# Kernel tuning notes

Measured on AMD Instinct MI355X. Metric: run time of the kernel, lower is better.

The kernel has to match this reference:

```python
import jax, jax.numpy as jnp
import numpy as np

NUM_SCALES = 3
LAMBDA_0 = 1.0
MU_0 = 1.0
KAPPA_LAMBDA = 0.5
KAPPA_MU = 0.5
BASE_WEIGHT = 1.0
GRADIENT_SCALING = 0.1


def tgradient(f, axis):
    """torch.gradient semantics: central diff interior, one-sided at edges (spacing=1)."""
    n = f.shape[axis]
    def sl(a, b):
        idx = [slice(None)] * f.ndim
        idx[axis] = slice(a, b)
        return f[tuple(idx)]
    interior = (sl(2, n) - sl(0, n - 2)) * 0.5
    first = sl(1, 2) - sl(0, 1)
    last = sl(n - 1, n) - sl(n - 2, n - 1)
    return jnp.concatenate([first, interior, last], axis=axis)


def resize1d_linear(x, axis, out_size):
    """1D linear resize along `axis` with align_corners=True."""
    in_size = x.shape[axis]
    if out_size == in_size:
        return x
    denom = max(out_size - 1, 1)
    coords = jnp.arange(out_size, dtype=jnp.float32) * ((in_size - 1) / denom)
    i0 = jnp.floor(coords).astype(jnp.int32)
    i1 = jnp.minimum(i0 + 1, in_size - 1)
    w = (coords - i0.astype(jnp.float32)).astype(x.dtype)
    shape = [1] * x.ndim
    shape[axis] = out_size
    w = w.reshape(shape)
    x0 = jnp.take(x, i0, axis=axis)
    x1 = jnp.take(x, i1, axis=axis)
    return x0 * (1 - w) + x1 * w


def trilinear_downsample(x, scale):
    # F.interpolate(..., scale_factor=1/scale, mode='trilinear', align_corners=True,
    # recompute_scale_factor=True): out_size = floor(in_size / scale); separable linear.
    for axis in (2, 3, 4):
        out_size = int(np.floor(x.shape[axis] / scale))
        x = resize1d_linear(x, axis, out_size)
    return x


def elasticity_loss(deformation_field, image):
    total_loss = jnp.float32(0.0)
    for i in range(NUM_SCALES):
        scale = 2 ** i
        deform = trilinear_downsample(deformation_field, scale)
        img = trilinear_downsample(image, scale)
        u, v, w = deform[:, 0], deform[:, 1], deform[:, 2]  # each (B, X, Y, Z)
        du_dx, du_dy, du_dz = tgradient(u, 1), tgradient(u, 2), tgradient(u, 3)
        dv_dx, dv_dy, dv_dz = tgradient(v, 1), tgradient(v, 2), tgradient(v, 3)
        dw_dx, dw_dy, dw_dz = tgradient(w, 1), tgradient(w, 2), tgradient(w, 3)
        E_xx, E_yy, E_zz = du_dx, dv_dy, dw_dz
        E_xy = 0.5 * (du_dy + dv_dx)
        E_xz = 0.5 * (du_dz + dw_dx)
        E_yz = 0.5 * (dv_dz + dw_dy)
        trace_E = E_xx + E_yy + E_zz
        ic = img[:, 0]  # (B, X, Y, Z)
        gx, gy, gz = tgradient(ic, 1), tgradient(ic, 2), tgradient(ic, 3)
        image_gradient = jnp.sqrt(gx * gx + gy * gy + gz * gz)
        adaptive_lambda = LAMBDA_0 + KAPPA_LAMBDA * image_gradient
        adaptive_mu = MU_0 + KAPPA_MU * image_gradient
        elastic_energy = (0.5 * adaptive_lambda * trace_E ** 2
                          + adaptive_mu * (E_xx ** 2 + E_yy ** 2 + E_zz ** 2
                                           + 2.0 * (E_xy ** 2 + E_xz ** 2 + E_yz ** 2)))
        adaptive_weight = BASE_WEIGHT + GRADIENT_SCALING * image_gradient
        total_loss = total_loss + jnp.mean(adaptive_weight * elastic_energy)
    return total_loss


def setup_inputs() -> dict:
    key = jax.random.key(0)
    k1, k2 = jax.random.split(key)
    deformation_field = jax.random.normal(k1, (2, 3, 160, 192, 160), dtype=jnp.float32)
    image = jax.random.uniform(k2, (2, 1, 160, 192, 160), dtype=jnp.float32)
    return {"deformation_field": deformation_field, "image": image}


def reference(deformation_field, image):
    return elasticity_loss(deformation_field, image)
```

## Files before the change

kernel.cpp:

```cpp
#include <hip/hip_runtime.h>
#include <math.h>


#define LAMBDA_0 1.0f
#define MU_0 1.0f
#define KAPPA_LAMBDA 0.5f
#define KAPPA_MU 0.5f
#define BASE_WEIGHT 1.0f
#define GRADIENT_SCALING 0.1f

typedef float v4f __attribute__((ext_vector_type(4)));

constexpr int S_TY = 32;
constexpr int S_TZ = 32;
constexpr int S_CX = 8;

__global__ __launch_bounds__(256, 2)
void elasticity_stream_reg2_kernel(const float* __restrict__ def,
                                   const float* __restrict__ img,
                                   int X, int Y, int Z,
                                   int nby, int nbz, int nbx,
                                   float inv_n, float* __restrict__ out) {
    int t = blockIdx.x;
    const int bx = t % nbx; t /= nbx;
    const int bz = t % nbz; t /= nbz;
    const int by = t % nby; t /= nby;
    const int b = t;

    const int tid = threadIdx.x;
    const int zg = tid & 7;
    const int ly = tid >> 3;
    const int lane = tid & 63;
    const int laneM = (lane - 1) & 63;
    const int laneP = (lane + 1) & 63;

    const long long vol = (long long)X * Y * Z;
    const long long sX = (long long)Y * Z;
    const float* __restrict__ p0 = def + ((long long)b * 3 + 0) * vol;
    const float* __restrict__ p1 = def + ((long long)b * 3 + 1) * vol;
    const float* __restrict__ p2 = def + ((long long)b * 3 + 2) * vol;
    const float* __restrict__ p3 = img + (long long)b * vol;

    const int gy = by * S_TY + ly;
    const int gz0 = bz * S_TZ + 4 * zg;
    const int x0 = bx * S_CX;

    const long long offC  = (long long)gy * Z + gz0;
    const long long offYm = (long long)max(gy - 1, 0) * Z + gz0;
    const long long offYp = (long long)min(gy + 1, Y - 1) * Z + gz0;
    const long long offZm = offC - ((gz0 > 0) ? 1 : 0);
    const long long offZp = offC + ((gz0 + 4 < Z) ? 4 : 3);

    const bool ylo = (gy == 0), yhi = (gy == Y - 1);
    const bool zlo = (gz0 == 0), zhi = (gz0 + 4 == Z);
    const bool zem = (zg == 0),  zep = (zg == 7);

    v4f pc[4], cc[4], nc[4];
    {
        const long long o_ = (long long)max(x0 - 1, 0) * sX;
        pc[0] = *(const v4f*)(p0 + o_ + offC);
        pc[1] = *(const v4f*)(p1 + o_ + offC);
        pc[2] = *(const v4f*)(p2 + o_ + offC);
        pc[3] = *(const v4f*)(p3 + o_ + offC);
    }
    {
        const long long o_ = (long long)x0 * sX;
        cc[0] = *(const v4f*)(p0 + o_ + offC);
        cc[1] = *(const v4f*)(p1 + o_ + offC);
        cc[2] = *(const v4f*)(p2 + o_ + offC);
        cc[3] = *(const v4f*)(p3 + o_ + offC);
    }

    float acc = 0.f;
#pragma unroll 2
    for (int i = 0; i < S_CX; ++i) {
        const int x = x0 + i;
        const bool xlo = (x == 0), xhi = (x == X - 1);
        const long long oC = (long long)x * sX;
        const long long oN = (long long)min(x + 1, X - 1) * sX;

        nc[0] = *(const v4f*)(p0 + oN + offC);
        nc[1] = *(const v4f*)(p1 + oN + offC);
        nc[2] = *(const v4f*)(p2 + oN + offC);
        nc[3] = *(const v4f*)(p3 + oN + offC);

        v4f ym[4], yp[4];
        ym[0] = *(const v4f*)(p0 + oC + offYm);
        ym[1] = *(const v4f*)(p1 + oC + offYm);
        ym[2] = *(const v4f*)(p2 + oC + offYm);
        ym[3] = *(const v4f*)(p3 + oC + offYm);
        yp[0] = *(const v4f*)(p0 + oC + offYp);
        yp[1] = *(const v4f*)(p1 + oC + offYp);
        yp[2] = *(const v4f*)(p2 + oC + offYp);
        yp[3] = *(const v4f*)(p3 + oC + offYp);

        float zmS[4] = {0.f, 0.f, 0.f, 0.f};
        float zpS[4] = {0.f, 0.f, 0.f, 0.f};
        if (zem) {
            zmS[0] = p0[oC + offZm]; zmS[1] = p1[oC + offZm];
            zmS[2] = p2[oC + offZm]; zmS[3] = p3[oC + offZm];
        }
        if (zep) {
            zpS[0] = p0[oC + offZp]; zpS[1] = p1[oC + offZp];
            zpS[2] = p2[oC + offZp]; zpS[3] = p3[oC + offZp];
        }

        v4f gxA[4], gyA[4], gzA[4];
#pragma unroll
        for (int f = 0; f < 4; ++f) {
            v4f c = cc[f];
            gxA[f] = xlo ? (nc[f] - c)
                         : (xhi ? (c - pc[f]) : 0.5f * (nc[f] - pc[f]));
            gyA[f] = ylo ? (yp[f] - c)
                         : (yhi ? (c - ym[f]) : 0.5f * (yp[f] - ym[f]));
            float zmv = __shfl(c[3], laneM, 64);
            float zpv = __shfl(c[0], laneP, 64);
            float zm = zem ? zmS[f] : zmv;
            float zp = zep ? zpS[f] : zpv;
            v4f gz;
            gz[0] = zlo ? (c[1] - c[0]) : 0.5f * (c[1] - zm);
            gz[1] = 0.5f * (c[2] - c[0]);
            gz[2] = 0.5f * (c[3] - c[1]);
            gz[3] = zhi ? (c[3] - c[2]) : 0.5f * (zp - c[2]);
            gzA[f] = gz;
        }

#pragma unroll
        for (int j = 0; j < 4; ++j) {
            float Exx = gxA[0][j], Eyy = gyA[1][j], Ezz = gzA[2][j];
            float Exy = 0.5f * (gyA[0][j] + gxA[1][j]);
            float Exz = 0.5f * (gzA[0][j] + gxA[2][j]);
            float Eyz = 0.5f * (gzA[1][j] + gyA[2][j]);
            float tr = Exx + Eyy + Ezz;
            float g = sqrtf(gxA[3][j] * gxA[3][j] + gyA[3][j] * gyA[3][j] +
                            gzA[3][j] * gzA[3][j]);
            float lam = LAMBDA_0 + KAPPA_LAMBDA * g;
            float mu  = MU_0 + KAPPA_MU * g;
            float energy = 0.5f * lam * tr * tr +
                           mu * (Exx * Exx + Eyy * Eyy + Ezz * Ezz +
                                 2.0f * (Exy * Exy + Exz * Exz + Eyz * Eyz));
            acc += (BASE_WEIGHT + GRADIENT_SCALING * g) * energy;
        }

#pragma unroll
        for (int f = 0; f < 4; ++f) { pc[f] = cc[f]; cc[f] = nc[f]; }
    }

    float val = acc * inv_n;
    for (int off = 32; off > 0; off >>= 1)
        val += __shfl_down(val, off, 64);
    __shared__ float smem[4];
    const int wid = (int)(threadIdx.x >> 6);
    if ((threadIdx.x & 63) == 0) smem[wid] = val;
    __syncthreads();
    if (threadIdx.x == 0)
        atomicAdd(out, smem[0] + smem[1] + smem[2] + smem[3]);
}


__global__ void downsample3d_kernel(const float* __restrict__ in,
                                    float* __restrict__ out,
                                    int nmaps,
                                    int inX, int inY, int inZ,
                                    int outX, int outY, int outZ,
                                    float rx, float ry, float rz) {
    long long total = (long long)nmaps * outX * outY * outZ;
    long long idx = (long long)blockIdx.x * blockDim.x + threadIdx.x;
    if (idx >= total) return;

    int z = (int)(idx % outZ);
    long long t = idx / outZ;
    int y = (int)(t % outY);
    t /= outY;
    int x = (int)(t % outX);
    int m = (int)(t / outX);

    float cx = (float)x * rx;
    float cy = (float)y * ry;
    float cz = (float)z * rz;
    int ix0 = (int)floorf(cx), iy0 = (int)floorf(cy), iz0 = (int)floorf(cz);
    float wx = cx - (float)ix0, wy = cy - (float)iy0, wz = cz - (float)iz0;
    int ix1 = min(ix0 + 1, inX - 1);
    int iy1 = min(iy0 + 1, inY - 1);
    int iz1 = min(iz0 + 1, inZ - 1);

    long long sYZ = (long long)inY * inZ;
    const float* p = in + (long long)m * inX * sYZ;

    long long bx0 = (long long)ix0 * sYZ, bx1 = (long long)ix1 * sYZ;
    long long by0 = (long long)iy0 * inZ, by1 = (long long)iy1 * inZ;

    float v000 = p[bx0 + by0 + iz0], v001 = p[bx0 + by0 + iz1];
    float v010 = p[bx0 + by1 + iz0], v011 = p[bx0 + by1 + iz1];
    float v100 = p[bx1 + by0 + iz0], v101 = p[bx1 + by0 + iz1];
    float v110 = p[bx1 + by1 + iz0], v111 = p[bx1 + by1 + iz1];

    float a00 = v000 * (1.f - wx) + v100 * wx;
    float a01 = v001 * (1.f - wx) + v101 * wx;
    float a10 = v010 * (1.f - wx) + v110 * wx;
    float a11 = v011 * (1.f - wx) + v111 * wx;
    float b0 = a00 * (1.f - wy) + a10 * wy;
    float b1 = a01 * (1.f - wy) + a11 * wy;
    out[idx] = b0 * (1.f - wz) + b1 * wz;
}

__global__ void elasticity_loss_v4_kernel(const float* __restrict__ def,
                                          const float* __restrict__ img,
                                          int B, int X, int Y, int Z,
                                          float inv_n,
                                          float* __restrict__ out) {
    const int Zg = Z >> 2;
    long long total = (long long)B * X * Y * Zg;
    long long idx = (long long)blockIdx.x * blockDim.x + threadIdx.x;
    float val = 0.f;
    if (idx < total) {
        int zg = (int)(idx % Zg);
        long long t = idx / Zg;
        int y = (int)(t % Y);
        t /= Y;
        int x = (int)(t % X);
        int b = (int)(t / X);
        int z0 = zg << 2;

        long long vol = (long long)X * Y * Z;
        const float* base0 = def + ((long long)b * 3 + 0) * vol;
        const float* base1 = def + ((long long)b * 3 + 1) * vol;
        const float* base2 = def + ((long long)b * 3 + 2) * vol;
        const float* base3 = img + (long long)b * vol;
        const float* bases[4] = {base0, base1, base2, base3};

        long long sX = (long long)Y * Z;
        long long c = (long long)x * sX + (long long)y * Z + z0;
        long long cxm = (x > 0) ? c - sX : c;
        long long cxp = (x < X - 1) ? c + sX : c;
        long long cym = (y > 0) ? c - Z : c;
        long long cyp = (y < Y - 1) ? c + Z : c;
        long long czm = (z0 > 0) ? c - 1 : c;
        long long czp = (z0 + 4 < Z) ? c + 4 : c;

        float C[4][4], XM[4][4], XP[4][4], YM[4][4], YP[4][4];
        float ZM[4], ZP[4];
#pragma unroll
        for (int f = 0; f < 4; ++f) {
            const float* p = bases[f];
            float4 tc = *(const float4*)(p + c);
            float4 txm = *(const float4*)(p + cxm);
            float4 txp = *(const float4*)(p + cxp);
            float4 tym = *(const float4*)(p + cym);
            float4 typ = *(const float4*)(p + cyp);
            ZM[f] = p[czm];
            ZP[f] = p[czp];
            C[f][0] = tc.x;  C[f][1] = tc.y;  C[f][2] = tc.z;  C[f][3] = tc.w;
            XM[f][0] = txm.x; XM[f][1] = txm.y; XM[f][2] = txm.z; XM[f][3] = txm.w;
            XP[f][0] = txp.x; XP[f][1] = txp.y; XP[f][2] = txp.z; XP[f][3] = txp.w;
            YM[f][0] = tym.x; YM[f][1] = tym.y; YM[f][2] = tym.z; YM[f][3] = tym.w;
            YP[f][0] = typ.x; YP[f][1] = typ.y; YP[f][2] = typ.z; YP[f][3] = typ.w;
        }

        const bool xlo = (x == 0), xhi = (x == X - 1);
        const bool ylo = (y == 0), yhi = (y == Y - 1);
        const bool zlo = (z0 == 0), zhi = (z0 + 4 == Z);

        float GX[4][4], GY[4][4], GZ[4][4];
#pragma unroll
        for (int f = 0; f < 4; ++f) {
#pragma unroll
            for (int i = 0; i < 4; ++i) {
                GX[f][i] = xlo ? (XP[f][i] - C[f][i])
                               : (xhi ? (C[f][i] - XM[f][i])
                                      : 0.5f * (XP[f][i] - XM[f][i]));
                GY[f][i] = ylo ? (YP[f][i] - C[f][i])
                               : (yhi ? (C[f][i] - YM[f][i])
                                      : 0.5f * (YP[f][i] - YM[f][i]));
            }
            GZ[f][0] = zlo ? (C[f][1] - C[f][0]) : 0.5f * (C[f][1] - ZM[f]);
            GZ[f][1] = 0.5f * (C[f][2] - C[f][0]);
            GZ[f][2] = 0.5f * (C[f][3] - C[f][1]);
            GZ[f][3] = zhi ? (C[f][3] - C[f][2]) : 0.5f * (ZP[f] - C[f][2]);
        }

        float acc = 0.f;
#pragma unroll
        for (int i = 0; i < 4; ++i) {
            float Exx = GX[0][i], Eyy = GY[1][i], Ezz = GZ[2][i];
            float Exy = 0.5f * (GY[0][i] + GX[1][i]);
            float Exz = 0.5f * (GZ[0][i] + GX[2][i]);
            float Eyz = 0.5f * (GZ[1][i] + GY[2][i]);
            float tr = Exx + Eyy + Ezz;
            float g = sqrtf(GX[3][i] * GX[3][i] + GY[3][i] * GY[3][i] +
                            GZ[3][i] * GZ[3][i]);
            float lam = LAMBDA_0 + KAPPA_LAMBDA * g;
            float mu  = MU_0 + KAPPA_MU * g;
            float energy = 0.5f * lam * tr * tr +
                           mu * (Exx * Exx + Eyy * Eyy + Ezz * Ezz +
                                 2.0f * (Exy * Exy + Exz * Exz + Eyz * Eyz));
            float wgt = BASE_WEIGHT + GRADIENT_SCALING * g;
            acc += wgt * energy;
        }
        val = acc * inv_n;
    }

    for (int off = 32; off > 0; off >>= 1)
        val += __shfl_down(val, off, 64);
    __shared__ float smem[8];
    int lane = threadIdx.x & 63;
    int wid = (int)(threadIdx.x >> 6);
    if (lane == 0) smem[wid] = val;
    __syncthreads();
    if (threadIdx.x == 0) {
        float s = 0.f;
        int nw = (int)(blockDim.x >> 6);
        for (int i = 0; i < nw; ++i) s += smem[i];
        atomicAdd(out, s);
    }
}

static void launch_loss_v4(const float* def, const float* img, int B, int X,
                           int Y, int Z, float* out, hipStream_t stream) {
    const int BLOCK = 256;
    long long nvox = (long long)B * X * Y * Z;
    long long total = nvox >> 2;
    float inv_n = (float)(1.0 / (double)nvox);
    int grid = (int)((total + BLOCK - 1) / BLOCK);
    elasticity_loss_v4_kernel<<<grid, BLOCK, 0, stream>>>(def, img, B, X, Y, Z,
                                                          inv_n, out);
}

extern "C" void kernel_launch(void* const* d_in, const int* in_sizes, int n_in,
                              void* d_out, int out_size, void* d_ws, size_t ws_size,
                              hipStream_t stream) {
    const float* def = (const float*)d_in[0];
    const float* img = (const float*)d_in[1];
    float* out = (float*)d_out;

    const int B = 2;
    const int X0 = 160, Y0 = 192, Z0 = 160;

    hipMemsetAsync(out, 0, sizeof(float), stream);

    const int BLOCK = 256;

    {
        long long nvox = (long long)B * X0 * Y0 * Z0;
        float inv_n = (float)(1.0 / (double)nvox);
        int nby = Y0 / S_TY;
        int nbz = Z0 / S_TZ;
        int nbx = X0 / S_CX;
        int grid = B * nby * nbz * nbx;
        elasticity_stream_reg2_kernel<<<grid, 256, 0, stream>>>(def, img,
                                                                X0, Y0, Z0,
                                                                nby, nbz, nbx,
                                                                inv_n, out);
    }

    const int X2 = 80, Y2 = 96, Z2 = 80;
    const int X4 = 40, Y4 = 48, Z4 = 40;
    long long vol2 = (long long)X2 * Y2 * Z2;
    long long vol4 = (long long)X4 * Y4 * Z4;

    float* def2 = (float*)d_ws;
    float* img2 = def2 + (long long)B * 3 * vol2;
    float* def4 = img2 + (long long)B * vol2;
    float* img4 = def4 + (long long)B * 3 * vol4;

    {
        float rx = (float)((double)(X0 - 1) / (double)(X2 - 1));
        float ry = (float)((double)(Y0 - 1) / (double)(Y2 - 1));
        float rz = (float)((double)(Z0 - 1) / (double)(Z2 - 1));
        long long td = (long long)B * 3 * vol2;
        int gd = (int)((td + BLOCK - 1) / BLOCK);
        downsample3d_kernel<<<gd, BLOCK, 0, stream>>>(def, def2, B * 3,
                                                      X0, Y0, Z0, X2, Y2, Z2,
                                                      rx, ry, rz);
        long long ti = (long long)B * vol2;
        int gi = (int)((ti + BLOCK - 1) / BLOCK);
        downsample3d_kernel<<<gi, BLOCK, 0, stream>>>(img, img2, B,
                                                      X0, Y0, Z0, X2, Y2, Z2,
                                                      rx, ry, rz);
        launch_loss_v4(def2, img2, B, X2, Y2, Z2, out, stream);
    }

    {
        float rx = (float)((double)(X0 - 1) / (double)(X4 - 1));
        float ry = (float)((double)(Y0 - 1) / (double)(Y4 - 1));
        float rz = (float)((double)(Z0 - 1) / (double)(Z4 - 1));
        long long td = (long long)B * 3 * vol4;
        int gd = (int)((td + BLOCK - 1) / BLOCK);
        downsample3d_kernel<<<gd, BLOCK, 0, stream>>>(def, def4, B * 3,
                                                      X0, Y0, Z0, X4, Y4, Z4,
                                                      rx, ry, rz);
        long long ti = (long long)B * vol4;
        int gi = (int)((ti + BLOCK - 1) / BLOCK);
        downsample3d_kernel<<<gi, BLOCK, 0, stream>>>(img, img4, B,
                                                      X0, Y0, Z0, X4, Y4, Z4,
                                                      rx, ry, rz);
        launch_loss_v4(def4, img4, B, X4, Y4, Z4, out, stream);
    }
}
```

Before: 134.8 us.

## Merge downsample launches, swizzle workgroups across XCDs, enlarge x-chunk

Result: faster. 121.9 us (-9.6%).

```diff
diff --git a/kernel.cpp b/kernel.cpp
--- a/kernel.cpp
+++ b/kernel.cpp
@@ -13,15 +13,18 @@
 
 constexpr int S_TY = 32;
 constexpr int S_TZ = 32;
-constexpr int S_CX = 8;
+constexpr int S_CX = 10;
 
 __global__ __launch_bounds__(256, 2)
-void elasticity_stream_reg2_kernel(const float* __restrict__ def,
-                                   const float* __restrict__ img,
-                                   int X, int Y, int Z,
-                                   int nby, int nbz, int nbx,
-                                   float inv_n, float* __restrict__ out) {
-    int t = blockIdx.x;
+void elasticity_stream_reg2s_kernel(const float* __restrict__ def,
+                                    const float* __restrict__ img,
+                                    int X, int Y, int Z,
+                                    int nby, int nbz, int nbx,
+                                    int nwg,
+                                    float inv_n, float* __restrict__ out) {
+    const int cpx = nwg >> 3;
+    int t = (blockIdx.x % 8) * cpx + (blockIdx.x / 8);
+
     const int bx = t % nbx; t /= nbx;
     const int bz = t % nbz; t /= nbz;
     const int by = t % nby; t /= nby;
@@ -157,23 +160,30 @@
         atomicAdd(out, smem[0] + smem[1] + smem[2] + smem[3]);
 }
 
-
-__global__ void downsample3d_kernel(const float* __restrict__ in,
-                                    float* __restrict__ out,
-                                    int nmaps,
-                                    int inX, int inY, int inZ,
-                                    int outX, int outY, int outZ,
-                                    float rx, float ry, float rz) {
-    long long total = (long long)nmaps * outX * outY * outZ;
+__global__ void downsample_all8_kernel(const float* __restrict__ def,
+                                       const float* __restrict__ img,
+                                       float* __restrict__ odef,
+                                       float* __restrict__ oimg,
+                                       int inX, int inY, int inZ,
+                                       int outX, int outY, int outZ,
+                                       float rx, float ry, float rz) {
+    long long pervol = (long long)outX * outY * outZ;
+    long long total = 8LL * pervol;
     long long idx = (long long)blockIdx.x * blockDim.x + threadIdx.x;
     if (idx >= total) return;
 
-    int z = (int)(idx % outZ);
-    long long t = idx / outZ;
+    int m = (int)(idx / pervol);
+    long long r = idx % pervol;
+    int z = (int)(r % outZ);
+    long long t = r / outZ;
     int y = (int)(t % outY);
-    t /= outY;
-    int x = (int)(t % outX);
-    int m = (int)(t / outX);
+    int x = (int)(t / outY);
+
+    long long invol = (long long)inX * inY * inZ;
+    const float* src;
+    float* dst;
+    if (m < 6) { src = def + (long long)m * invol;       dst = odef + (long long)m * pervol; }
+    else       { src = img + (long long)(m - 6) * invol; dst = oimg + (long long)(m - 6) * pervol; }
 
     float cx = (float)x * rx;
     float cy = (float)y * ry;
@@ -185,15 +195,13 @@
     int iz1 = min(iz0 + 1, inZ - 1);
 
     long long sYZ = (long long)inY * inZ;
-    const float* p = in + (long long)m * inX * sYZ;
-
     long long bx0 = (long long)ix0 * sYZ, bx1 = (long long)ix1 * sYZ;
     long long by0 = (long long)iy0 * inZ, by1 = (long long)iy1 * inZ;
 
-    float v000 = p[bx0 + by0 + iz0], v001 = p[bx0 + by0 + iz1];
-    float v010 = p[bx0 + by1 + iz0], v011 = p[bx0 + by1 + iz1];
-    float v100 = p[bx1 + by0 + iz0], v101 = p[bx1 + by0 + iz1];
-    float v110 = p[bx1 + by1 + iz0], v111 = p[bx1 + by1 + iz1];
+    float v000 = src[bx0 + by0 + iz0], v001 = src[bx0 + by0 + iz1];
+    float v010 = src[bx0 + by1 + iz0], v011 = src[bx0 + by1 + iz1];
+    float v100 = src[bx1 + by0 + iz0], v101 = src[bx1 + by0 + iz1];
+    float v110 = src[bx1 + by1 + iz0], v111 = src[bx1 + by1 + iz1];
 
     float a00 = v000 * (1.f - wx) + v100 * wx;
     float a01 = v001 * (1.f - wx) + v101 * wx;
@@ -201,7 +209,7 @@
     float a11 = v011 * (1.f - wx) + v111 * wx;
     float b0 = a00 * (1.f - wy) + a10 * wy;
     float b1 = a01 * (1.f - wy) + a11 * wy;
-    out[idx] = b0 * (1.f - wz) + b1 * wz;
+    dst[r] = b0 * (1.f - wz) + b1 * wz;
 }
 
 __global__ void elasticity_loss_v4_kernel(const float* __restrict__ def,
@@ -336,7 +344,7 @@
     const int B = 2;
     const int X0 = 160, Y0 = 192, Z0 = 160;
 
-    hipMemsetAsync(out, 0, sizeof(float), stream);
+    (void)hipMemsetAsync(out, 0, sizeof(float), stream);
 
     const int BLOCK = 256;
 
@@ -346,10 +354,11 @@
         int nby = Y0 / S_TY;
         int nbz = Z0 / S_TZ;
         int nbx = X0 / S_CX;
-        int grid = B * nby * nbz * nbx;
-        elasticity_stream_reg2_kernel<<<grid, 256, 0, stream>>>(def, img,
+        int nwg = B * nby * nbz * nbx;
+        elasticity_stream_reg2s_kernel<<<nwg, 256, 0, stream>>>(def, img,
                                                                 X0, Y0, Z0,
                                                                 nby, nbz, nbx,
+                                                                nwg,
                                                                 inv_n, out);
     }
 
@@ -367,16 +376,11 @@
         float rx = (float)((double)(X0 - 1) / (double)(X2 - 1));
         float ry = (float)((double)(Y0 - 1) / (double)(Y2 - 1));
         float rz = (float)((double)(Z0 - 1) / (double)(Z2 - 1));
-        long long td = (long long)B * 3 * vol2;
-        int gd = (int)((td + BLOCK - 1) / BLOCK);
-        downsample3d_kernel<<<gd, BLOCK, 0, stream>>>(def, def2, B * 3,
-                                                      X0, Y0, Z0, X2, Y2, Z2,
-                                                      rx, ry, rz);
-        long long ti = (long long)B * vol2;
-        int gi = (int)((ti + BLOCK - 1) / BLOCK);
-        downsample3d_kernel<<<gi, BLOCK, 0, stream>>>(img, img2, B,
-                                                      X0, Y0, Z0, X2, Y2, Z2,
-                                                      rx, ry, rz);
+        long long total = 8LL * vol2;
+        int g = (int)((total + BLOCK - 1) / BLOCK);
+        downsample_all8_kernel<<<g, BLOCK, 0, stream>>>(def, img, def2, img2,
+                                                        X0, Y0, Z0, X2, Y2, Z2,
+                                                        rx, ry, rz);
         launch_loss_v4(def2, img2, B, X2, Y2, Z2, out, stream);
     }
 
@@ -384,16 +388,11 @@
         float rx = (float)((double)(X0 - 1) / (double)(X4 - 1));
         float ry = (float)((double)(Y0 - 1) / (double)(Y4 - 1));
         float rz = (float)((double)(Z0 - 1) / (double)(Z4 - 1));
-        long long td = (long long)B * 3 * vol4;
-        int gd = (int)((td + BLOCK - 1) / BLOCK);
-        downsample3d_kernel<<<gd, BLOCK, 0, stream>>>(def, def4, B * 3,
-                                                      X0, Y0, Z0, X4, Y4, Z4,
-                                                      rx, ry, rz);
-        long long ti = (long long)B * vol4;
-        int gi = (int)((ti + BLOCK - 1) / BLOCK);
-        downsample3d_kernel<<<gi, BLOCK, 0, stream>>>(img, img4, B,
-                                                      X0, Y0, Z0, X4, Y4, Z4,
-                                                      rx, ry, rz);
+        long long total = 8LL * vol4;
+        int g = (int)((total + BLOCK - 1) / BLOCK);
+        downsample_all8_kernel<<<g, BLOCK, 0, stream>>>(def, img, def4, img4,
+                                                        X0, Y0, Z0, X4, Y4, Z4,
+                                                        rx, ry, rz);
         launch_loss_v4(def4, img4, B, X4, Y4, Z4, out, stream);
     }
 }
```
